# Performance work log

Hardware: AMD Instinct MI355X
Metric: run time of the kernel (lower is better)

## Reference

```python
import jax, jax.numpy as jnp
import numpy as np

EPS = 1e-8  # torch CosineSimilarity eps
V_FD = 2.0


def _tstudent(cos):
    # (1 + (1/v)*(1 - cos))^(-(v+1)/2)
    return (1.0 + (1.0 / V_FD) * (1.0 - cos)) ** (-(V_FD + 1.0) / 2.0)


def setup_inputs() -> dict:
    key = jax.random.key(0)
    k1, k2 = jax.random.split(key)
    z1 = jax.random.normal(k1, (8192, 768), dtype=jnp.float32)
    z2 = jax.random.normal(k2, (8192, 768), dtype=jnp.float32)
    return {"z1": z1, "z2": z2}


def reference(z1, z2):
    # L2-normalize rows (clamped norm as in torch.nn.CosineSimilarity)
    n1 = z1 / jnp.maximum(jnp.linalg.norm(z1, axis=-1, keepdims=True), EPS)
    n2 = z2 / jnp.maximum(jnp.linalg.norm(z2, axis=-1, keepdims=True), EPS)
    # full pairwise cosine matrix [N, N] computed once (replaces per-row loop)
    cos_mat = jnp.einsum('nd,md->nm', n1, n2)
    # numerator: matched-pair similarities == diagonal of cos_mat
    num = _tstudent(jnp.diagonal(cos_mat))
    # denominator: row-sum of t-Student kernel over all pairs
    denom = jnp.sum(_tstudent(cos_mat), axis=1)
    return -jnp.mean(num / denom)
```

## Files before the change

kernel.cpp:

```cpp
#include <hip/hip_runtime.h>
#include <hip/hip_bf16.h>
#include <stdint.h>

#define N_ROWS 8192
#define DIM    768
#define BM     256
#define BN     256
#define BKB    128
#define KTILES (DIM / BKB)
#define NT2    (N_ROWS / BN)
#define LDS_BYTES 131072

typedef __attribute__((ext_vector_type(4)))  int   i32x4;
typedef __attribute__((ext_vector_type(4)))  float f32x4;

__device__ __forceinline__ float tstudent(float c) {
    float t = 1.5f - 0.5f * c;
    float r = rsqrtf(t);
    return r * r * r;
}

__global__ __launch_bounds__(256) void norm_kernel(const float* __restrict__ z1,
                                                   const float* __restrict__ z2,
                                                   signed char* __restrict__ n1,
                                                   signed char* __restrict__ n2,
                                                   float* __restrict__ num,
                                                   float* __restrict__ inva,
                                                   float* __restrict__ invb) {
    int row = blockIdx.x;
    int t = threadIdx.x;
    const float* s1 = z1 + (size_t)row * DIM;
    const float* s2 = z2 + (size_t)row * DIM;
    float a0 = s1[t], a1 = s1[t + 256], a2 = s1[t + 512];
    float b0 = s2[t], b1 = s2[t + 256], b2 = s2[t + 512];
    float ss1 = a0 * a0 + a1 * a1 + a2 * a2;
    float ss2 = b0 * b0 + b1 * b1 + b2 * b2;
    float sd  = a0 * b0 + a1 * b1 + a2 * b2;
    for (int off = 32; off; off >>= 1) {
        ss1 += __shfl_down(ss1, off);
        ss2 += __shfl_down(ss2, off);
        sd  += __shfl_down(sd, off);
    }
    __shared__ float w1[4], w2[4], wd[4];
    __shared__ float sc1_s, sc2_s;
    if ((t & 63) == 0) { int wi = t >> 6; w1[wi] = ss1; w2[wi] = ss2; wd[wi] = sd; }
    __syncthreads();
    if (t == 0) {
        float nrm1 = fmaxf(sqrtf(w1[0] + w1[1] + w1[2] + w1[3]), 1e-8f);
        float nrm2 = fmaxf(sqrtf(w2[0] + w2[1] + w2[2] + w2[3]), 1e-8f);
        float dot  = wd[0] + wd[1] + wd[2] + wd[3];
        sc1_s = 127.0f / nrm1;
        sc2_s = 127.0f / nrm2;
        num[row] = tstudent(dot / (nrm1 * nrm2));
    }
    __syncthreads();
    float sc1 = sc1_s, sc2 = sc2_s;
    float qa0 = fminf(fmaxf(rintf(a0 * sc1), -127.f), 127.f);
    float qa1 = fminf(fmaxf(rintf(a1 * sc1), -127.f), 127.f);
    float qa2 = fminf(fmaxf(rintf(a2 * sc1), -127.f), 127.f);
    float qb0 = fminf(fmaxf(rintf(b0 * sc2), -127.f), 127.f);
    float qb1 = fminf(fmaxf(rintf(b1 * sc2), -127.f), 127.f);
    float qb2 = fminf(fmaxf(rintf(b2 * sc2), -127.f), 127.f);
    signed char* d1 = n1 + (size_t)row * DIM;
    signed char* d2 = n2 + (size_t)row * DIM;
    d1[t]       = (signed char)(int)qa0;
    d1[t + 256] = (signed char)(int)qa1;
    d1[t + 512] = (signed char)(int)qa2;
    d2[t]       = (signed char)(int)qb0;
    d2[t + 256] = (signed char)(int)qb1;
    d2[t + 512] = (signed char)(int)qb2;
    float sq1 = qa0 * qa0 + qa1 * qa1 + qa2 * qa2;
    float sq2 = qb0 * qb0 + qb1 * qb1 + qb2 * qb2;
    for (int off = 32; off; off >>= 1) {
        sq1 += __shfl_down(sq1, off);
        sq2 += __shfl_down(sq2, off);
    }
    __shared__ float wq1[4], wq2[4];
    if ((t & 63) == 0) { int wi = t >> 6; wq1[wi] = sq1; wq2[wi] = sq2; }
    __syncthreads();
    if (t == 0) {
        inva[row] = rsqrtf(wq1[0] + wq1[1] + wq1[2] + wq1[3]);
        invb[row] = rsqrtf(wq2[0] + wq2[1] + wq2[2] + wq2[3]);
    }
}


__device__ __forceinline__ void stG(const signed char* g, char* lds, int t, int j) {
    __builtin_amdgcn_global_load_lds(
        (const __attribute__((address_space(1))) void*)(g + (size_t)j * 128 * DIM),
        (__attribute__((address_space(3))) void*)(lds + t * 16 + j * 16384), 16, 0, 0);
}

#define BAR()  asm volatile("s_barrier" ::: "memory")
#define VMW(n) asm volatile("s_waitcnt vmcnt(" #n ")" ::: "memory")

#define HALFK(SEG)                                                              \
    {                                                                           \
        i32x4 b0 = *(const i32x4*)(Bb + rbB + 0 * 2048 + (SEG));                \
        i32x4 b1 = *(const i32x4*)(Bb + rbB + 1 * 2048 + (SEG));                \
        i32x4 b2 = *(const i32x4*)(Bb + rbB + 2 * 2048 + (SEG));                \
        i32x4 b3 = *(const i32x4*)(Bb + rbB + 3 * 2048 + (SEG));                \
        _Pragma("unroll")                                                       \
        for (int m = 0; m < 4; ++m) {                                           \
            i32x4 a = *(const i32x4*)(Ab + rbA + m * 2048 + (SEG));             \
            __builtin_amdgcn_s_setprio(1);                                      \
            acc[m][0] = __builtin_amdgcn_mfma_i32_16x16x64_i8(a, b0, acc[m][0], 0, 0, 0); \
            acc[m][1] = __builtin_amdgcn_mfma_i32_16x16x64_i8(a, b1, acc[m][1], 0, 0, 0); \
            acc[m][2] = __builtin_amdgcn_mfma_i32_16x16x64_i8(a, b2, acc[m][2], 0, 0, 0); \
            acc[m][3] = __builtin_amdgcn_mfma_i32_16x16x64_i8(a, b3, acc[m][3], 0, 0, 0); \
            __builtin_amdgcn_s_setprio(0);                                      \
        }                                                                       \
    }

__global__ __launch_bounds__(1024) void gemm_kernel(const signed char* __restrict__ n1,
                                                    const signed char* __restrict__ n2,
                                                    const float* __restrict__ inva,
                                                    const float* __restrict__ invb,
                                                    float* __restrict__ partial) {
    extern __shared__ char smem[];
    int t = threadIdx.x;
    int l = t & 63;
    int w = t >> 6;
    int wr = w >> 2;
    int wc = w & 3;

    int bid = blockIdx.x;
    int xcd = bid & 7, idx = bid >> 3;
    int br = xcd * 4 + (idx & 3);
    int bc = (idx >> 4) * 4 + ((idx >> 2) & 3);
    int rowbase = br * BM, colbase = bc * BN;

    int sr = t >> 3;
    int gcol0 = ((t & 7) ^ (sr & 7)) * 16;
    const signed char* Ag = n1 + (size_t)(rowbase + sr) * DIM + gcol0;
    const signed char* Bg = n2 + (size_t)(colbase + sr) * DIM + gcol0;

    i32x4 acc[4][4] = {};

    int seg0 = (((l >> 4) + 0) ^ (l & 7)) * 16;
    int seg1 = (((l >> 4) + 4) ^ (l & 7)) * 16;
    int rbA = (wr * 64 + (l & 15)) * 128;
    int rbB = (wc * 64 + (l & 15)) * 128;

    stG(Ag, smem, t, 0);         stG(Ag, smem, t, 1);
    stG(Bg, smem + 65536, t, 0); stG(Bg, smem + 65536, t, 1);
    VMW(0); BAR();

    #pragma unroll
    for (int kt = 0; kt < KTILES - 1; ++kt) {
        int db = kt & 1;
        const char* Ab = smem + db * 32768;
        const char* Bb = smem + 65536 + db * 32768;
        char* AnW = smem + (db ^ 1) * 32768;
        char* BnW = smem + 65536 + (db ^ 1) * 32768;
        const signed char* Agn = Ag + (kt + 1) * BKB;
        const signed char* Bgn = Bg + (kt + 1) * BKB;

        stG(Agn, AnW, t, 0); stG(Agn, AnW, t, 1);
        stG(Bgn, BnW, t, 0); stG(Bgn, BnW, t, 1);
        HALFK(seg0);
        HALFK(seg1);
        VMW(0); BAR();
    }
    {
        const char* Ab = smem + 32768;
        const char* Bb = smem + 65536 + 32768;
        HALFK(seg0);
        HALFK(seg1);
    }

    float invb_n[4];
    #pragma unroll
    for (int n = 0; n < 4; ++n)
        invb_n[n] = invb[colbase + wc * 64 + n * 16 + (l & 15)];

    float* red = (float*)smem;
    __syncthreads();
    #pragma unroll
    for (int m = 0; m < 4; ++m) {
        f32x4 ia = *(const f32x4*)(inva + rowbase + wr * 64 + m * 16 + (l >> 4) * 4);
        #pragma unroll
        for (int j = 0; j < 4; ++j) {
            float s = 0.f;
            #pragma unroll
            for (int n = 0; n < 4; ++n) {
                float cos = (float)acc[m][n][j] * ia[j] * invb_n[n];
                s += tstudent(cos);
            }
            s += __shfl_xor(s, 1);
            s += __shfl_xor(s, 2);
            s += __shfl_xor(s, 4);
            s += __shfl_xor(s, 8);
            if ((l & 15) == 0) {
                int row = wr * 64 + m * 16 + (l >> 4) * 4 + j;
                red[row * 4 + wc] = s;
            }
        }
    }
    __syncthreads();
    if (t < BM) {
        partial[(size_t)bc * N_ROWS + rowbase + t] = red[t * 4 + 0] + red[t * 4 + 1] + red[t * 4 + 2] + red[t * 4 + 3];
    }
}

__global__ __launch_bounds__(256) void reduce_kernel(const float* __restrict__ partial,
                                                     const float* __restrict__ num,
                                                     float* __restrict__ blocksum) {
    int row = blockIdx.x * 256 + threadIdx.x;
    float d = 0.f;
    #pragma unroll 8
    for (int ct = 0; ct < NT2; ++ct) d += partial[(size_t)ct * N_ROWS + row];
    float s = num[row] / d;
    for (int off = 32; off; off >>= 1) s += __shfl_down(s, off);
    __shared__ float wsum[4];
    if ((threadIdx.x & 63) == 0) wsum[threadIdx.x >> 6] = s;
    __syncthreads();
    if (threadIdx.x == 0) blocksum[blockIdx.x] = wsum[0] + wsum[1] + wsum[2] + wsum[3];
}

__global__ __launch_bounds__(64) void final_kernel(const float* __restrict__ blocksum,
                                                   float* __restrict__ out) {
    int l = threadIdx.x;
    float s = (l < 32) ? blocksum[l] : 0.f;
    for (int off = 32; off; off >>= 1) s += __shfl_down(s, off);
    if (l == 0) out[0] = -(s / (float)N_ROWS);
}

extern "C" void kernel_launch(void* const* d_in, const int* in_sizes, int n_in,
                              void* d_out, int out_size, void* d_ws, size_t ws_size,
                              hipStream_t stream) {
    const float* z1 = (const float*)d_in[0];
    const float* z2 = (const float*)d_in[1];
    char* ws = (char*)d_ws;
    const size_t n_bytes = (size_t)N_ROWS * DIM;
    signed char* n1 = (signed char*)ws;
    signed char* n2 = (signed char*)(ws + n_bytes);
    size_t base2 = 2 * n_bytes;
    float* num      = (float*)(ws + base2);
    float* inva     = (float*)(ws + base2 + 32768);
    float* invb     = (float*)(ws + base2 + 65536);
    float* partial  = (float*)(ws + base2 + 98304);
    float* blocksum = (float*)(ws + base2 + 98304 + 2097152);

    hipFuncSetAttribute((const void*)gemm_kernel,
                        hipFuncAttributeMaxDynamicSharedMemorySize, LDS_BYTES);

    norm_kernel<<<N_ROWS, 256, 0, stream>>>(z1, z2, n1, n2, num, inva, invb);
    gemm_kernel<<<NT2 * NT2, 1024, LDS_BYTES, stream>>>(n1, n2, inva, invb, partial);
    reduce_kernel<<<N_ROWS / 256, 256, 0, stream>>>(partial, num, blocksum);
    final_kernel<<<1, 64, 0, stream>>>(blocksum, (float*)d_out);
}
```

Baseline: 88.50 us.

## Load A operand directly from global into registers, stage only B in LDS

The A tile is no longer staged through LDS. Each wave reads its A fragments straight from global memory into registers inside the MFMA loop, and only the B tile is double-buffered in LDS, which halves LDS usage. This removes the LDS write and read traffic for A and could allow more occupancy. In exchange, global load latency now sits directly in the MFMA dependency chain, and waves that share rows issue redundant global reads. The s_waitcnt vmcnt(0) barrier also now waits for the A loads.

Result: slower. 150.4 us (+70.0%).

```diff
diff --git a/kernel.cpp b/kernel.cpp
--- a/kernel.cpp
+++ b/kernel.cpp
@@ -9,7 +9,7 @@
 #define BKB    128
 #define KTILES (DIM / BKB)
 #define NT2    (N_ROWS / BN)
-#define LDS_BYTES 131072
+#define LDS_BYTES 65536
 
 typedef __attribute__((ext_vector_type(4)))  int   i32x4;
 typedef __attribute__((ext_vector_type(4)))  float f32x4;
@@ -94,22 +94,34 @@
 #define BAR()  asm volatile("s_barrier" ::: "memory")
 #define VMW(n) asm volatile("s_waitcnt vmcnt(" #n ")" ::: "memory")
 
-#define HALFK(SEG)                                                              \
+#define HALFK(SEG, GOFF)                                                        \
     {                                                                           \
         i32x4 b0 = *(const i32x4*)(Bb + rbB + 0 * 2048 + (SEG));                \
         i32x4 b1 = *(const i32x4*)(Bb + rbB + 1 * 2048 + (SEG));                \
         i32x4 b2 = *(const i32x4*)(Bb + rbB + 2 * 2048 + (SEG));                \
         i32x4 b3 = *(const i32x4*)(Bb + rbB + 3 * 2048 + (SEG));                \
-        _Pragma("unroll")                                                       \
-        for (int m = 0; m < 4; ++m) {                                           \
-            i32x4 a = *(const i32x4*)(Ab + rbA + m * 2048 + (SEG));             \
-            __builtin_amdgcn_s_setprio(1);                                      \
-            acc[m][0] = __builtin_amdgcn_mfma_i32_16x16x64_i8(a, b0, acc[m][0], 0, 0, 0); \
-            acc[m][1] = __builtin_amdgcn_mfma_i32_16x16x64_i8(a, b1, acc[m][1], 0, 0, 0); \
-            acc[m][2] = __builtin_amdgcn_mfma_i32_16x16x64_i8(a, b2, acc[m][2], 0, 0, 0); \
-            acc[m][3] = __builtin_amdgcn_mfma_i32_16x16x64_i8(a, b3, acc[m][3], 0, 0, 0); \
-            __builtin_amdgcn_s_setprio(0);                                      \
-        }                                                                       \
+        i32x4 a0 = *(const i32x4*)(Aw + (GOFF));                                \
+        i32x4 a1 = *(const i32x4*)(Aw + 12288 + (GOFF));                        \
+        i32x4 a2 = *(const i32x4*)(Aw + 24576 + (GOFF));                        \
+        i32x4 a3 = *(const i32x4*)(Aw + 36864 + (GOFF));                        \
+        __builtin_amdgcn_s_setprio(1);                                          \
+        acc[0][0] = __builtin_amdgcn_mfma_i32_16x16x64_i8(a0, b0, acc[0][0], 0, 0, 0); \
+        acc[0][1] = __builtin_amdgcn_mfma_i32_16x16x64_i8(a0, b1, acc[0][1], 0, 0, 0); \
+        acc[0][2] = __builtin_amdgcn_mfma_i32_16x16x64_i8(a0, b2, acc[0][2], 0, 0, 0); \
+        acc[0][3] = __builtin_amdgcn_mfma_i32_16x16x64_i8(a0, b3, acc[0][3], 0, 0, 0); \
+        acc[1][0] = __builtin_amdgcn_mfma_i32_16x16x64_i8(a1, b0, acc[1][0], 0, 0, 0); \
+        acc[1][1] = __builtin_amdgcn_mfma_i32_16x16x64_i8(a1, b1, acc[1][1], 0, 0, 0); \
+        acc[1][2] = __builtin_amdgcn_mfma_i32_16x16x64_i8(a1, b2, acc[1][2], 0, 0, 0); \
+        acc[1][3] = __builtin_amdgcn_mfma_i32_16x16x64_i8(a1, b3, acc[1][3], 0, 0, 0); \
+        acc[2][0] = __builtin_amdgcn_mfma_i32_16x16x64_i8(a2, b0, acc[2][0], 0, 0, 0); \
+        acc[2][1] = __builtin_amdgcn_mfma_i32_16x16x64_i8(a2, b1, acc[2][1], 0, 0, 0); \
+        acc[2][2] = __builtin_amdgcn_mfma_i32_16x16x64_i8(a2, b2, acc[2][2], 0, 0, 0); \
+        acc[2][3] = __builtin_amdgcn_mfma_i32_16x16x64_i8(a2, b3, acc[2][3], 0, 0, 0); \
+        acc[3][0] = __builtin_amdgcn_mfma_i32_16x16x64_i8(a3, b0, acc[3][0], 0, 0, 0); \
+        acc[3][1] = __builtin_amdgcn_mfma_i32_16x16x64_i8(a3, b1, acc[3][1], 0, 0, 0); \
+        acc[3][2] = __builtin_amdgcn_mfma_i32_16x16x64_i8(a3, b2, acc[3][2], 0, 0, 0); \
+        acc[3][3] = __builtin_amdgcn_mfma_i32_16x16x64_i8(a3, b3, acc[3][3], 0, 0, 0); \
+        __builtin_amdgcn_s_setprio(0);                                          \
     }
 
 __global__ __launch_bounds__(1024) void gemm_kernel(const signed char* __restrict__ n1,
@@ -132,41 +144,35 @@
 
     int sr = t >> 3;
     int gcol0 = ((t & 7) ^ (sr & 7)) * 16;
-    const signed char* Ag = n1 + (size_t)(rowbase + sr) * DIM + gcol0;
     const signed char* Bg = n2 + (size_t)(colbase + sr) * DIM + gcol0;
+
+    const signed char* Aw = n1 + (size_t)(rowbase + wr * 64 + (l & 15)) * DIM + (l >> 4) * 16;
 
     i32x4 acc[4][4] = {};
 
     int seg0 = (((l >> 4) + 0) ^ (l & 7)) * 16;
     int seg1 = (((l >> 4) + 4) ^ (l & 7)) * 16;
-    int rbA = (wr * 64 + (l & 15)) * 128;
     int rbB = (wc * 64 + (l & 15)) * 128;
 
-    stG(Ag, smem, t, 0);         stG(Ag, smem, t, 1);
-    stG(Bg, smem + 65536, t, 0); stG(Bg, smem + 65536, t, 1);
+    stG(Bg, smem, t, 0); stG(Bg, smem, t, 1);
     VMW(0); BAR();
 
     #pragma unroll
     for (int kt = 0; kt < KTILES - 1; ++kt) {
         int db = kt & 1;
-        const char* Ab = smem + db * 32768;
-        const char* Bb = smem + 65536 + db * 32768;
-        char* AnW = smem + (db ^ 1) * 32768;
-        char* BnW = smem + 65536 + (db ^ 1) * 32768;
-        const signed char* Agn = Ag + (kt + 1) * BKB;
+        const char* Bb = smem + db * 32768;
+        char* BnW = smem + (db ^ 1) * 32768;
         const signed char* Bgn = Bg + (kt + 1) * BKB;
 
-        stG(Agn, AnW, t, 0); stG(Agn, AnW, t, 1);
         stG(Bgn, BnW, t, 0); stG(Bgn, BnW, t, 1);
-        HALFK(seg0);
-        HALFK(seg1);
+        HALFK(seg0, kt * 128);
+        HALFK(seg1, kt * 128 + 64);
         VMW(0); BAR();
     }
     {
-        const char* Ab = smem + 32768;
-        const char* Bb = smem + 65536 + 32768;
-        HALFK(seg0);
-        HALFK(seg1);
+        const char* Bb = smem + 32768;
+        HALFK(seg0, 5 * 128);
+        HALFK(seg1, 5 * 128 + 64);
     }
 
     float invb_n[4];
```
